# Kernel tuning notes

Hardware: AMD Instinct MI355X
Metric: run time of the kernel (lower is better)

The kernel has to match this reference:

```python
import jax
import jax.numpy as jnp
from jax import lax
import numpy as np

# module hyperparameters (match init_kwargs)
IN_C, OUT_C = 32, 64
K, STRIDE, PAD, DIL = 3, 1, 1, 1
GRID_SIZE, ORDER = 5, 3
GRID_LO, GRID_HI = -1.0, 1.0
SCALE_SPLINE = 1.0
EPS = 1e-8


def _knot_grid():
    # grid = arange(-order, grid_size+order+1) * h + lo ; length = grid_size + 2*order + 1 = 12
    h = (GRID_HI - GRID_LO) / GRID_SIZE
    return jnp.arange(-ORDER, GRID_SIZE + ORDER + 1, dtype=jnp.float32) * h + GRID_LO


def _bspline_bases(x):
    """Cox-de Boor recursion. x: (N, P) -> bases: (N, P, GRID_SIZE+ORDER)."""
    grid = _knot_grid()
    xe = x[..., None]  # (N, P, 1)
    bases = ((xe >= grid[:-1]) & (xe < grid[1:])).astype(x.dtype)  # (N, P, 11)
    for k in range(1, ORDER + 1):
        left_den = jnp.maximum(grid[k:-1] - grid[:-(k + 1)], EPS)
        right_den = jnp.maximum(grid[k + 1:] - grid[1:-k], EPS)
        bases = ((xe - grid[:-(k + 1)]) / left_den * bases[..., :-1]
                 + (grid[k + 1:] - xe) / right_den * bases[..., 1:])
    return bases  # (N, P, 8)


def setup_inputs() -> dict:
    key = jax.random.key(0)
    k1, k2, k3 = jax.random.split(key, 3)
    x = jax.random.normal(k1, (4, IN_C, 56, 56), dtype=jnp.float32)
    base_weight = jax.random.normal(k2, (OUT_C, IN_C, K, K), dtype=jnp.float32) * 0.05
    spline_weight = jax.random.normal(k3, (OUT_C, IN_C * K * K, GRID_SIZE + ORDER), dtype=jnp.float32) * 0.05
    spline_scaler = jnp.ones((OUT_C,), dtype=jnp.float32)
    return {"x": x, "base_weight": base_weight,
            "spline_weight": spline_weight, "spline_scaler": spline_scaler}


def reference(x, base_weight, spline_weight, spline_scaler):
    B, C, H, W = x.shape
    pad = [(PAD, PAD), (PAD, PAD)]
    # base path: conv2d -> SiLU
    base_conv = lax.conv_general_dilated(
        x, base_weight, window_strides=(STRIDE, STRIDE), padding=pad,
        rhs_dilation=(DIL, DIL), dimension_numbers=("NCHW", "OIHW", "NCHW"))
    base_out = jax.nn.silu(base_conv)

    # unfold: (B, C*K*K, oh, ow) with torch Unfold channel ordering (c, kh, kw)
    patches = lax.conv_general_dilated_patches(
        x, filter_shape=(K, K), window_strides=(STRIDE, STRIDE), padding=pad,
        rhs_dilation=(DIL, DIL))
    oh, ow = patches.shape[2], patches.shape[3]
    num_patches = oh * ow
    # (B*num_patches, C*K*K)
    pf = patches.reshape(B, C * K * K, num_patches).transpose(0, 2, 1).reshape(-1, C * K * K)

    bases = _bspline_bases(pf)  # (N, P, F)
    # contract patch-dim and basis-dim against spline weights
    spl = jnp.einsum("npf,opf->no", bases, spline_weight) * spline_scaler  # (N, O)
    spl = spl.reshape(B, num_patches, OUT_C).transpose(0, 2, 1).reshape(B, OUT_C, oh, ow)
    return base_out + SCALE_SPLINE * spl
```

## Files before the change

### kernel.cpp

```cpp
#include <hip/hip_runtime.h>
#include <math.h>


typedef __attribute__((ext_vector_type(8))) short bf16x8;
typedef __attribute__((ext_vector_type(4))) float f32x4;

#define MFMA16(a, b, c) __builtin_amdgcn_mfma_f32_16x16x32_bf16((a), (b), (c), 0, 0, 0)

__device__ __forceinline__ unsigned short f2bf(float f) {
    unsigned u = __builtin_bit_cast(unsigned, f);
    u = (u + 0x7fffu + ((u >> 16) & 1u)) >> 16;
    return (unsigned short)u;
}

__device__ __forceinline__ void eval_bases(float v, float bs[8]) {
    #pragma unroll
    for (int i = 0; i < 8; ++i) bs[i] = 0.0f;
    float t = (v + 2.2f) * 2.5f;
    if (t >= 0.0f && t < 11.0f) {
        int j = (int)t;
        if (j > 10) j = 10;
        float knot = (float)(j - 3) * 0.4f - 1.0f;
        float u  = (v - knot) * 2.5f;
        float um = 1.0f - u;
        float u2 = u * u, u3 = u2 * u;
        const float s6 = 1.0f / 6.0f;
        float w0 = um * um * um * s6;
        float w1 = (3.0f * u3 - 6.0f * u2 + 4.0f) * s6;
        float w2 = (-3.0f * u3 + 3.0f * u2 + 3.0f * u + 1.0f) * s6;
        float w3 = u3 * s6;
        int i0 = j - 3;
        if (i0 >= 0)               bs[i0]     = w0;
        if (i0 + 1 >= 0 && i0 < 7) bs[i0 + 1] = w1;
        if (i0 + 2 >= 0 && i0 < 6) bs[i0 + 2] = w2;
        if (i0 + 3 <= 7)           bs[i0 + 3] = w3;
    }
}

__global__ __launch_bounds__(256)
void cvt_swz_kernel(const float* __restrict__ ws, const float* __restrict__ wb,
                    unsigned short* __restrict__ wst, unsigned short* __restrict__ wbt) {
    int i = blockIdx.x * 256 + threadIdx.x;
    if (i < 147456) {
        int j = i & 7, l = (i >> 3) & 63, t = i >> 9;
        int S = t % 72, nq = t / 72;
        int oc = nq * 16 + (l & 15);
        int k  = S * 32 + (l >> 4) * 8 + j;
        wst[i] = f2bf(ws[oc * 2304 + k]);
    } else {
        int i2 = i - 147456;
        if (i2 < 18432) {
            int j = i2 & 7, l = (i2 >> 3) & 63, t = i2 >> 9;
            int s = t % 9, nq = t / 9;
            int oc = nq * 16 + (l & 15);
            int c  = (l >> 4) * 8 + j;
            wbt[i2] = f2bf(wb[oc * 288 + c * 9 + s]);
        }
    }
}

__global__ __launch_bounds__(512)
void kan_mfma_kernel(const float* __restrict__ x,
                     const float* __restrict__ sc,
                     const unsigned short* __restrict__ wst,
                     const unsigned short* __restrict__ wbt,
                     float* __restrict__ out) {
    __shared__ unsigned short smem[29600];
    unsigned short* sb = smem;
    unsigned short* xh = smem + 25600;

    const int tid = threadIdx.x;
    const int bx  = blockIdx.x;
    const int b   = bx / 49;
    const int r   = bx - b * 49;
    const int ty  = r / 7;
    const int tx  = r - ty * 7;
    const int h0  = ty * 8, w0 = tx * 8;

    const int lane = tid & 63;
    const int wv   = tid >> 6;
    const int nq   = wv & 3;
    const int kh   = wv >> 2;
    const int ml   = lane & 15;
    const int kg   = lane >> 4;
    const int py0  = ml >> 3, px0 = ml & 7;

    float vv[7];
    #pragma unroll
    for (int j = 0; j < 7; ++j) {
        int i = tid + j * 512;
        float val = 0.0f;
        if (i < 3200) {
            int c  = i / 100;
            int hp = i - c * 100;
            int hy = hp / 10;
            int hx = hp - hy * 10;
            int hh = h0 + hy - 1, ww = w0 + hx - 1;
            if ((unsigned)hh < 56u && (unsigned)ww < 56u)
                val = x[((b * 32 + c) * 56 + hh) * 56 + ww];
        }
        vv[j] = val;
    }
    #pragma unroll
    for (int j = 0; j < 7; ++j) {
        int i = tid + j * 512;
        if (i < 3200) {
            int c  = i / 100;
            int hp = i - c * 100;
            float bs[8];
            eval_bases(vv[j], bs);
            bf16x8 pk;
            #pragma unroll
            for (int j2 = 0; j2 < 8; ++j2) pk[j2] = (short)f2bf(bs[j2]);
            *reinterpret_cast<bf16x8*>(&sb[i * 8]) = pk;
            xh[hp * 40 + c] = f2bf(vv[j]);
        }
    }

    const unsigned short* bp = wst + ((nq * 72 + kh * 36) * 64 + lane) * 8;
    bf16x8 bwbuf[2][9];
    #pragma unroll
    for (int u = 0; u < 9; ++u)
        bwbuf[0][u] = *reinterpret_cast<const bf16x8*>(bp + u * 512);

    const int sbeg = kh ? 5 : 0;
    const int nST  = kh ? 4 : 5;
    bf16x8 bbv[5];
    {
        const unsigned short* bbp = wbt + (nq * 9 * 64 + lane) * 8;
        #pragma unroll
        for (int s = 0; s < 5; ++s)
            if (s < nST)
                bbv[s] = *reinterpret_cast<const bf16x8*>(bbp + (sbeg + s) * 512);
    }

    __syncthreads();

    int aoff[9];
    #pragma unroll
    for (int u = 0; u < 9; ++u) {
        int tt  = 4 * u + kg;
        int dc  = tt / 9;
        int tap = tt - dc * 9;
        int th  = tap / 3;
        int tw  = tap - th * 3;
        aoff[u] = (dc * 100 + (py0 + th) * 10 + (px0 + tw)) * 8;
    }

    f32x4 aS[4] = {{0,0,0,0},{0,0,0,0},{0,0,0,0},{0,0,0,0}};
    f32x4 aB[4] = {{0,0,0,0},{0,0,0,0},{0,0,0,0},{0,0,0,0}};

    #pragma unroll
    for (int g = 0; g < 4; ++g) {
        const int cur = g & 1;
        if (g < 3) {
            #pragma unroll
            for (int u = 0; u < 9; ++u)
                bwbuf[cur ^ 1][u] =
                    *reinterpret_cast<const bf16x8*>(bp + ((g + 1) * 9 + u) * 512);
        }
        const int cbase = kh * 12800 + g * 3200;
        #pragma unroll
        for (int u = 0; u < 9; ++u) {
            #pragma unroll
            for (int f = 0; f < 4; ++f) {
                bf16x8 a = *reinterpret_cast<const bf16x8*>(&sb[cbase + aoff[u] + f * 160]);
                aS[f] = MFMA16(a, bwbuf[cur][u], aS[f]);
            }
        }
    }

    #pragma unroll
    for (int s = 0; s < 5; ++s)
        if (s < nST) {
            const int tap = sbeg + s;
            const int th  = tap >= 6 ? 2 : (tap >= 3 ? 1 : 0);
            const int tw  = tap - 3 * th;
            const int xa  = ((py0 + th) * 10 + (px0 + tw)) * 40 + kg * 8;
            #pragma unroll
            for (int f = 0; f < 4; ++f) {
                bf16x8 a = *reinterpret_cast<const bf16x8*>(&xh[xa + f * 800]);
                aB[f] = MFMA16(a, bbv[s], aB[f]);
            }
        }

    __syncthreads();
    float* red = reinterpret_cast<float*>(smem);
    const int idx = nq * 64 + lane;
    if (kh) {
        #pragma unroll
        for (int f = 0; f < 4; ++f) {
            #pragma unroll
            for (int w = 0; w < 4; ++w) red[(f * 4 + w) * 260 + idx] = aS[f][w];
        }
        #pragma unroll
        for (int f = 0; f < 4; ++f) {
            #pragma unroll
            for (int w = 0; w < 4; ++w) red[((16 + f * 4) + w) * 260 + idx] = aB[f][w];
        }
    }
    __syncthreads();
    if (!kh) {
        #pragma unroll
        for (int f = 0; f < 4; ++f) {
            #pragma unroll
            for (int w = 0; w < 4; ++w) aS[f][w] += red[(f * 4 + w) * 260 + idx];
        }
        #pragma unroll
        for (int f = 0; f < 4; ++f) {
            #pragma unroll
            for (int w = 0; w < 4; ++w) aB[f][w] += red[((16 + f * 4) + w) * 260 + idx];
        }

        const int oc  = nq * 16 + ml;
        const float scv = sc[oc];
        #pragma unroll
        for (int f = 0; f < 4; ++f) {
            const int py  = f * 2 + (kg >> 1);
            const int pxb = (kg & 1) * 4;
            float* ob = out + ((b * 64 + oc) * 56 + h0 + py) * 56 + w0 + pxb;
            f32x4 res;
            #pragma unroll
            for (int reg = 0; reg < 4; ++reg) {
                float bv = aB[f][reg];
                float si = bv / (1.0f + __expf(-bv));
                res[reg] = si + scv * aS[f][reg];
            }
            *reinterpret_cast<f32x4*>(ob) = res;
        }
    }
}

extern "C" void kernel_launch(void* const* d_in, const int* in_sizes, int n_in,
                              void* d_out, int out_size, void* d_ws, size_t ws_size,
                              hipStream_t stream) {
    const float* x  = (const float*)d_in[0];
    const float* wb = (const float*)d_in[1];
    const float* ws = (const float*)d_in[2];
    const float* sc = (const float*)d_in[3];
    float* out = (float*)d_out;

    unsigned short* wst = (unsigned short*)d_ws;
    unsigned short* wbt = wst + 147456;

    cvt_swz_kernel<<<648, 256, 0, stream>>>(ws, wb, wst, wbt);
    kan_mfma_kernel<<<196, 512, 0, stream>>>(x, sc, wst, wbt, out);
}
```

Before: 73.61 us.

## Fuse weight conversion into main kernel with a grid-wide flag barrier

Removes the separate bf16 weight convert/swizzle launch. The first 162 blocks of the main kernel do that conversion themselves, and every block waits on per-producer release/acquire flags before loading the converted weights. The B-spline and input staging work runs before the barrier, so it can overlap the conversion and one launch is saved. The costs are a spin-wait on 162 flags per block and reliance on all blocks being co-resident. The flags are never reset, so on later calls the barrier passes immediately while the weights are being rewritten, which is a stale-flag race.

```diff
diff --git a/kernel.cpp b/kernel.cpp
--- a/kernel.cpp
+++ b/kernel.cpp
@@ -6,6 +6,9 @@
 typedef __attribute__((ext_vector_type(4))) float f32x4;
 
 #define MFMA16(a, b, c) __builtin_amdgcn_mfma_f32_16x16x32_bf16((a), (b), (c), 0, 0, 0)
+
+#define NPROD 162
+#define MAGIC 0x9E3779B1u
 
 __device__ __forceinline__ unsigned short f2bf(float f) {
     unsigned u = __builtin_bit_cast(unsigned, f);
@@ -37,34 +40,15 @@
     }
 }
 
-__global__ __launch_bounds__(256)
-void cvt_swz_kernel(const float* __restrict__ ws, const float* __restrict__ wb,
-                    unsigned short* __restrict__ wst, unsigned short* __restrict__ wbt) {
-    int i = blockIdx.x * 256 + threadIdx.x;
-    if (i < 147456) {
-        int j = i & 7, l = (i >> 3) & 63, t = i >> 9;
-        int S = t % 72, nq = t / 72;
-        int oc = nq * 16 + (l & 15);
-        int k  = S * 32 + (l >> 4) * 8 + j;
-        wst[i] = f2bf(ws[oc * 2304 + k]);
-    } else {
-        int i2 = i - 147456;
-        if (i2 < 18432) {
-            int j = i2 & 7, l = (i2 >> 3) & 63, t = i2 >> 9;
-            int s = t % 9, nq = t / 9;
-            int oc = nq * 16 + (l & 15);
-            int c  = (l >> 4) * 8 + j;
-            wbt[i2] = f2bf(wb[oc * 288 + c * 9 + s]);
-        }
-    }
-}
-
 __global__ __launch_bounds__(512)
-void kan_mfma_kernel(const float* __restrict__ x,
-                     const float* __restrict__ sc,
-                     const unsigned short* __restrict__ wst,
-                     const unsigned short* __restrict__ wbt,
-                     float* __restrict__ out) {
+void kan_fused_kernel(const float* __restrict__ x,
+                      const float* __restrict__ wb,
+                      const float* __restrict__ ws,
+                      const float* __restrict__ sc,
+                      unsigned short* __restrict__ wst,
+                      unsigned short* __restrict__ wbt,
+                      unsigned* __restrict__ flags,
+                      float* __restrict__ out) {
     __shared__ unsigned short smem[29600];
     unsigned short* sb = smem;
     unsigned short* xh = smem + 25600;
@@ -84,6 +68,27 @@
     const int ml   = lane & 15;
     const int kg   = lane >> 4;
     const int py0  = ml >> 3, px0 = ml & 7;
+
+    if (bx < NPROD) {
+        #pragma unroll
+        for (int e = 0; e < 2; ++e) {
+            int gid = bx * 1024 + e * 512 + tid;
+            if (gid < 147456) {
+                int j = gid & 7, l = (gid >> 3) & 63, t = gid >> 9;
+                int S = t % 72, q = t / 72;
+                int oc = q * 16 + (l & 15);
+                int k  = S * 32 + (l >> 4) * 8 + j;
+                wst[gid] = f2bf(ws[oc * 2304 + k]);
+            } else {
+                int i2 = gid - 147456;
+                int j = i2 & 7, l = (i2 >> 3) & 63, t = i2 >> 9;
+                int s = t % 9, q = t / 9;
+                int oc = q * 16 + (l & 15);
+                int c  = (l >> 4) * 8 + j;
+                wbt[i2] = f2bf(wb[oc * 288 + c * 9 + s]);
+            }
+        }
+    }
 
     float vv[7];
     #pragma unroll
@@ -117,6 +122,17 @@
         }
     }
 
+    __threadfence();
+    __syncthreads();
+    if (bx < NPROD && tid == 0)
+        __hip_atomic_store(&flags[bx], MAGIC, __ATOMIC_RELEASE, __HIP_MEMORY_SCOPE_AGENT);
+    if (tid < NPROD) {
+        while (__hip_atomic_load(&flags[tid], __ATOMIC_ACQUIRE, __HIP_MEMORY_SCOPE_AGENT) != MAGIC)
+            __builtin_amdgcn_s_sleep(1);
+    }
+    __syncthreads();
+    __threadfence();
+
     const unsigned short* bp = wst + ((nq * 72 + kh * 36) * 64 + lane) * 8;
     bf16x8 bwbuf[2][9];
     #pragma unroll
@@ -133,8 +149,6 @@
             if (s < nST)
                 bbv[s] = *reinterpret_cast<const bf16x8*>(bbp + (sbeg + s) * 512);
     }
-
-    __syncthreads();
 
     int aoff[9];
     #pragma unroll
@@ -242,7 +256,7 @@
 
     unsigned short* wst = (unsigned short*)d_ws;
     unsigned short* wbt = wst + 147456;
-
-    cvt_swz_kernel<<<648, 256, 0, stream>>>(ws, wb, wst, wbt);
-    kan_mfma_kernel<<<196, 512, 0, stream>>>(x, sc, wst, wbt, out);
-}
+    unsigned* flags = (unsigned*)((char*)d_ws + 331776);
+
+    kan_fused_kernel<<<196, 512, 0, stream>>>(x, wb, ws, sc, wst, wbt, flags, out);
+}
```

Result: slower. 130.4 us (+77.2%).

## Retile MFMA waves into 2x2 M/N register tiles and drop weight prefetch

Applied to the files above, without the earlier changes.

Reassigns the eight waves so each computes a 32-row by 32-channel tile (two A fragments times two weight fragments) instead of 64 rows by 16 channels. This halves LDS reads of basis fragments per MFMA. In exchange it doubles global weight-fragment loads per MFMA. The explicit double-buffered register prefetch of spline weights is removed, with loads now issued inline in the loop.

```diff
diff --git a/kernel.cpp b/kernel.cpp
--- a/kernel.cpp
+++ b/kernel.cpp
@@ -79,11 +79,13 @@
 
     const int lane = tid & 63;
     const int wv   = tid >> 6;
-    const int nq   = wv & 3;
-    const int kh   = wv >> 2;
+    const int nqq  = wv & 1;
+    const int kh   = (wv >> 1) & 1;
+    const int mh   = wv >> 2;
     const int ml   = lane & 15;
     const int kg   = lane >> 4;
-    const int py0  = ml >> 3, px0 = ml & 7;
+    const int py0  = mh * 4 + (ml >> 3);
+    const int px0  = ml & 7;
 
     float vv[7];
     #pragma unroll
@@ -116,24 +118,6 @@
             xh[hp * 40 + c] = f2bf(vv[j]);
         }
     }
-
-    const unsigned short* bp = wst + ((nq * 72 + kh * 36) * 64 + lane) * 8;
-    bf16x8 bwbuf[2][9];
-    #pragma unroll
-    for (int u = 0; u < 9; ++u)
-        bwbuf[0][u] = *reinterpret_cast<const bf16x8*>(bp + u * 512);
-
-    const int sbeg = kh ? 5 : 0;
-    const int nST  = kh ? 4 : 5;
-    bf16x8 bbv[5];
-    {
-        const unsigned short* bbp = wbt + (nq * 9 * 64 + lane) * 8;
-        #pragma unroll
-        for (int s = 0; s < 5; ++s)
-            if (s < nST)
-                bbv[s] = *reinterpret_cast<const bf16x8*>(bbp + (sbeg + s) * 512);
-    }
-
     __syncthreads();
 
     int aoff[9];
@@ -147,86 +131,105 @@
         aoff[u] = (dc * 100 + (py0 + th) * 10 + (px0 + tw)) * 8;
     }
 
-    f32x4 aS[4] = {{0,0,0,0},{0,0,0,0},{0,0,0,0},{0,0,0,0}};
-    f32x4 aB[4] = {{0,0,0,0},{0,0,0,0},{0,0,0,0},{0,0,0,0}};
-
-    #pragma unroll
+    f32x4 aS[2][2] = {{{0,0,0,0},{0,0,0,0}},{{0,0,0,0},{0,0,0,0}}};
+    f32x4 aB[2][2] = {{{0,0,0,0},{0,0,0,0}},{{0,0,0,0},{0,0,0,0}}};
+
+    const unsigned short* bp0 = wst + ((nqq * 2 * 72 + kh * 36) * 64 + lane) * 8;
+    const unsigned short* bp1 = bp0 + 36864;
     for (int g = 0; g < 4; ++g) {
-        const int cur = g & 1;
-        if (g < 3) {
-            #pragma unroll
-            for (int u = 0; u < 9; ++u)
-                bwbuf[cur ^ 1][u] =
-                    *reinterpret_cast<const bf16x8*>(bp + ((g + 1) * 9 + u) * 512);
-        }
         const int cbase = kh * 12800 + g * 3200;
         #pragma unroll
         for (int u = 0; u < 9; ++u) {
-            #pragma unroll
-            for (int f = 0; f < 4; ++f) {
-                bf16x8 a = *reinterpret_cast<const bf16x8*>(&sb[cbase + aoff[u] + f * 160]);
-                aS[f] = MFMA16(a, bwbuf[cur][u], aS[f]);
+            const int so = (g * 9 + u) * 512;
+            bf16x8 bw0 = *reinterpret_cast<const bf16x8*>(bp0 + so);
+            bf16x8 bw1 = *reinterpret_cast<const bf16x8*>(bp1 + so);
+            bf16x8 a0  = *reinterpret_cast<const bf16x8*>(&sb[cbase + aoff[u]]);
+            bf16x8 a1  = *reinterpret_cast<const bf16x8*>(&sb[cbase + aoff[u] + 160]);
+            aS[0][0] = MFMA16(a0, bw0, aS[0][0]);
+            aS[0][1] = MFMA16(a0, bw1, aS[0][1]);
+            aS[1][0] = MFMA16(a1, bw0, aS[1][0]);
+            aS[1][1] = MFMA16(a1, bw1, aS[1][1]);
+        }
+    }
+
+    {
+        const unsigned short* bbp0 = wbt + (nqq * 2 * 9 * 64 + lane) * 8;
+        const unsigned short* bbp1 = bbp0 + 4608;
+        const int sbeg = kh ? 5 : 0;
+        const int nST  = kh ? 4 : 5;
+        #pragma unroll
+        for (int s = 0; s < 5; ++s)
+            if (s < nST) {
+                const int tap = sbeg + s;
+                const int th  = tap >= 6 ? 2 : (tap >= 3 ? 1 : 0);
+                const int tw  = tap - 3 * th;
+                const int so  = tap * 512;
+                const int xa  = ((py0 + th) * 10 + (px0 + tw)) * 40 + kg * 8;
+                bf16x8 bw0 = *reinterpret_cast<const bf16x8*>(bbp0 + so);
+                bf16x8 bw1 = *reinterpret_cast<const bf16x8*>(bbp1 + so);
+                bf16x8 a0  = *reinterpret_cast<const bf16x8*>(&xh[xa]);
+                bf16x8 a1  = *reinterpret_cast<const bf16x8*>(&xh[xa + 800]);
+                aB[0][0] = MFMA16(a0, bw0, aB[0][0]);
+                aB[0][1] = MFMA16(a0, bw1, aB[0][1]);
+                aB[1][0] = MFMA16(a1, bw0, aB[1][0]);
+                aB[1][1] = MFMA16(a1, bw1, aB[1][1]);
             }
-        }
-    }
-
-    #pragma unroll
-    for (int s = 0; s < 5; ++s)
-        if (s < nST) {
-            const int tap = sbeg + s;
-            const int th  = tap >= 6 ? 2 : (tap >= 3 ? 1 : 0);
-            const int tw  = tap - 3 * th;
-            const int xa  = ((py0 + th) * 10 + (px0 + tw)) * 40 + kg * 8;
-            #pragma unroll
-            for (int f = 0; f < 4; ++f) {
-                bf16x8 a = *reinterpret_cast<const bf16x8*>(&xh[xa + f * 800]);
-                aB[f] = MFMA16(a, bbv[s], aB[f]);
-            }
-        }
+    }
 
     __syncthreads();
     float* red = reinterpret_cast<float*>(smem);
-    const int idx = nq * 64 + lane;
+    const int idx = (mh * 2 + nqq) * 64 + lane;
     if (kh) {
         #pragma unroll
-        for (int f = 0; f < 4; ++f) {
-            #pragma unroll
-            for (int w = 0; w < 4; ++w) red[(f * 4 + w) * 260 + idx] = aS[f][w];
-        }
-        #pragma unroll
-        for (int f = 0; f < 4; ++f) {
-            #pragma unroll
-            for (int w = 0; w < 4; ++w) red[((16 + f * 4) + w) * 260 + idx] = aB[f][w];
-        }
+        for (int mi = 0; mi < 2; ++mi)
+            #pragma unroll
+            for (int ni = 0; ni < 2; ++ni)
+                #pragma unroll
+                for (int w = 0; w < 4; ++w)
+                    red[((mi * 2 + ni) * 4 + w) * 260 + idx] = aS[mi][ni][w];
+        #pragma unroll
+        for (int mi = 0; mi < 2; ++mi)
+            #pragma unroll
+            for (int ni = 0; ni < 2; ++ni)
+                #pragma unroll
+                for (int w = 0; w < 4; ++w)
+                    red[(16 + (mi * 2 + ni) * 4 + w) * 260 + idx] = aB[mi][ni][w];
     }
     __syncthreads();
     if (!kh) {
         #pragma unroll
-        for (int f = 0; f < 4; ++f) {
-            #pragma unroll
-            for (int w = 0; w < 4; ++w) aS[f][w] += red[(f * 4 + w) * 260 + idx];
-        }
-        #pragma unroll
-        for (int f = 0; f < 4; ++f) {
-            #pragma unroll
-            for (int w = 0; w < 4; ++w) aB[f][w] += red[((16 + f * 4) + w) * 260 + idx];
-        }
-
-        const int oc  = nq * 16 + ml;
-        const float scv = sc[oc];
-        #pragma unroll
-        for (int f = 0; f < 4; ++f) {
-            const int py  = f * 2 + (kg >> 1);
-            const int pxb = (kg & 1) * 4;
-            float* ob = out + ((b * 64 + oc) * 56 + h0 + py) * 56 + w0 + pxb;
-            f32x4 res;
-            #pragma unroll
-            for (int reg = 0; reg < 4; ++reg) {
-                float bv = aB[f][reg];
-                float si = bv / (1.0f + __expf(-bv));
-                res[reg] = si + scv * aS[f][reg];
+        for (int mi = 0; mi < 2; ++mi)
+            #pragma unroll
+            for (int ni = 0; ni < 2; ++ni)
+                #pragma unroll
+                for (int w = 0; w < 4; ++w)
+                    aS[mi][ni][w] += red[((mi * 2 + ni) * 4 + w) * 260 + idx];
+        #pragma unroll
+        for (int mi = 0; mi < 2; ++mi)
+            #pragma unroll
+            for (int ni = 0; ni < 2; ++ni)
+                #pragma unroll
+                for (int w = 0; w < 4; ++w)
+                    aB[mi][ni][w] += red[(16 + (mi * 2 + ni) * 4 + w) * 260 + idx];
+
+        #pragma unroll
+        for (int ni = 0; ni < 2; ++ni) {
+            const int oc  = nqq * 32 + ni * 16 + ml;
+            const float scv = sc[oc];
+            #pragma unroll
+            for (int mi = 0; mi < 2; ++mi) {
+                const int py  = mh * 4 + mi * 2 + (kg >> 1);
+                const int pxb = (kg & 1) * 4;
+                float* ob = out + ((b * 64 + oc) * 56 + h0 + py) * 56 + w0 + pxb;
+                f32x4 res;
+                #pragma unroll
+                for (int reg = 0; reg < 4; ++reg) {
+                    float bv = aB[mi][ni][reg];
+                    float si = bv / (1.0f + __expf(-bv));
+                    res[reg] = si + scv * aS[mi][ni][reg];
+                }
+                *reinterpret_cast<f32x4*>(ob) = res;
             }
-            *reinterpret_cast<f32x4*>(ob) = res;
         }
     }
 }
```

After: 76.91 us. +4.5%, slower.
